# Performance work log

Hardware: AMD Instinct MI355X
Metric: run time of the kernel (lower is better)

## Reference

```python
import jax, jax.numpy as jnp
import numpy as np

N_FEATURES = 170
D_MODEL = 64
N_HEADS = 4
ALPHA = 0.1
LN_EPS = 1e-5
LEAKY_SLOPE = 0.01  # torch F.leaky_relu default
N = 3 * N_FEATURES  # 510
B = 32


def setup_inputs() -> dict:
    key = jax.random.key(0)
    ks = jax.random.split(key, 10)
    D, H = D_MODEL, N_HEADS
    s = 1.0 / np.sqrt(D)
    return {
        "x": jax.random.normal(ks[0], (B, N, D), dtype=jnp.float32),
        "causal_graph": jax.random.uniform(ks[1], (N, N), dtype=jnp.float32),
        # nn.Linear(d_model, d_model*n_heads, bias=False): stored here as (D, H*D) for x @ W
        "W": jax.random.uniform(ks[2], (D, H * D), jnp.float32, -s, s),
        "attention_w": jax.random.normal(ks[3], (H, 2 * D), dtype=jnp.float32),
        # Conv2d(2, n_heads, 3, padding=1): OIHW kernel
        "conv_w": jax.random.uniform(ks[4], (H, 2, 3, 3), jnp.float32, -1/np.sqrt(18), 1/np.sqrt(18)),
        "conv_b": jax.random.uniform(ks[5], (H,), jnp.float32, -1/np.sqrt(18), 1/np.sqrt(18)),
        # nn.Linear(d_model, 2*d_model): stored as (D, 2D)
        "fcg_w": jax.random.uniform(ks[6], (D, 2 * D), jnp.float32, -s, s),
        "fcg_b": jax.random.uniform(ks[7], (2 * D,), jnp.float32, -s, s),
        "ln_g": jnp.ones((D,), jnp.float32),
        "ln_b": jnp.zeros((D,), jnp.float32),
    }


def reference(x, causal_graph, W, attention_w, conv_w, conv_b, fcg_w, fcg_b, ln_g, ln_b):
    Bz, Nn, D = x.shape
    H = N_HEADS
    # shared projection: (B, N, H, D)
    xt = (x @ W).reshape(Bz, Nn, H, D)
    # GAT-style additive scores: concat-dot decomposed into two dot products
    w1, w2 = attention_w[:, :D], attention_w[:, D:]  # each (H, D)
    s_i = jnp.einsum('bnhd,hd->bhn', xt, w1)  # source term
    s_j = jnp.einsum('bnhd,hd->bhn', xt, w2)  # target term
    e = s_i[:, :, :, None] + s_j[:, :, None, :]  # (B, H, N, N)
    A_eva = jnp.where(e >= 0, e, LEAKY_SLOPE * e)  # leaky_relu
    # fuse mean attention with causal graph via 3x3 conv
    A_mean = A_eva.mean(axis=1)  # (B, N, N)
    causal = jnp.broadcast_to(causal_graph[None], (Bz, Nn, Nn))
    stacked = jnp.stack([A_mean, causal], axis=1)  # (B, 2, N, N)
    A_st = jax.lax.conv_general_dilated(
        stacked, conv_w, window_strides=(1, 1), padding=((1, 1), (1, 1)),
        dimension_numbers=('NCHW', 'OIHW', 'NCHW'))
    A_st = A_st + conv_b[None, :, None, None]  # (B, H, N, N)
    A = jax.nn.softmax(ALPHA * A_eva + (1.0 - ALPHA) * A_st, axis=-1)
    # multi-head aggregation then head-mean
    out = jnp.einsum('bhnm,bmhd->bnhd', A, xt).mean(axis=2)  # (B, N, D)
    # GLU
    g = out @ fcg_w + fcg_b  # (B, N, 2D)
    a, b = g[..., :D], g[..., D:]
    glu = a * jax.nn.sigmoid(b)
    # residual + layernorm
    y = glu + x
    mu = y.mean(axis=-1, keepdims=True)
    var = ((y - mu) ** 2).mean(axis=-1, keepdims=True)
    y = (y - mu) * jax.lax.rsqrt(var + LN_EPS) * ln_g + ln_b
    return y, A
```

## Files before the change

### kernel.cpp

```cpp
#include <hip/hip_runtime.h>

#define Bz 32
#define Nn 510
#define Dd 64
#define Hh 4
#define HD_ 256
#define Kpad 512
#define ALPHA_ 0.1f
#define LNEPS 1e-5f
#define SLOPE 0.01f
#define NEG_INF -3.0e38f

typedef __attribute__((ext_vector_type(8))) short short8;
typedef __attribute__((ext_vector_type(4))) float floatx4;

__device__ inline float wredsum(float v) {
  #pragma unroll
  for (int off = 32; off; off >>= 1) v += __shfl_xor(v, off, 64);
  return v;
}
__device__ inline float wredmax(float v) {
  #pragma unroll
  for (int off = 32; off; off >>= 1) v = fmaxf(v, __shfl_xor(v, off, 64));
  return v;
}
__device__ inline unsigned short f2bf(float f) {
  unsigned int u = __float_as_uint(f);
  unsigned int r = (u + 0x7fffu + ((u >> 16) & 1u)) >> 16;
  return (unsigned short)r;
}

__global__ __launch_bounds__(256) void k1_xt(const float* __restrict__ x,
                                             const float* __restrict__ W,
                                             const float* __restrict__ attw,
                                             unsigned short* __restrict__ xtT,
                                             float* __restrict__ si,
                                             float* __restrict__ sj) {
  __shared__ float Wl[64][68];
  __shared__ float xr[32][68];
  __shared__ unsigned short st[64 * 33];
  const int t = threadIdx.x;
  const int rt = blockIdx.x;
  const int b = blockIdx.y;
  const int ch = blockIdx.z;
  #pragma unroll
  for (int k = 0; k < 4; k++) {
    int f = t + k * 256;
    int kr = f >> 4;
    int c = (f & 15) * 4;
    *(float4*)&Wl[kr][c] = *(const float4*)&W[kr * HD_ + ch * 64 + c];
  }
  #pragma unroll
  for (int k = 0; k < 2; k++) {
    int f = t + k * 256;
    int r = f >> 4;
    int c = (f & 15) * 4;
    int row = rt * 32 + r;
    float4 v = make_float4(0.f, 0.f, 0.f, 0.f);
    if (row < Nn) v = *(const float4*)&x[(b * Nn + row) * Dd + c];
    *(float4*)&xr[r][c] = v;
  }
  __syncthreads();
  const int tg = t >> 4;
  const int tc = t & 15;
  const int rb = tg * 2, c0 = tc * 4;
  float acc[2][4] = {};
  #pragma unroll
  for (int k4 = 0; k4 < 16; k4++) {
    float4 xv0 = *(float4*)&xr[rb][k4 * 4];
    float4 xv1 = *(float4*)&xr[rb + 1][k4 * 4];
    #pragma unroll
    for (int kk = 0; kk < 4; kk++) {
      float4 wv = *(float4*)&Wl[k4 * 4 + kk][c0];
      float xs0 = (&xv0.x)[kk];
      float xs1 = (&xv1.x)[kk];
      acc[0][0] = fmaf(xs0, wv.x, acc[0][0]);
      acc[0][1] = fmaf(xs0, wv.y, acc[0][1]);
      acc[0][2] = fmaf(xs0, wv.z, acc[0][2]);
      acc[0][3] = fmaf(xs0, wv.w, acc[0][3]);
      acc[1][0] = fmaf(xs1, wv.x, acc[1][0]);
      acc[1][1] = fmaf(xs1, wv.y, acc[1][1]);
      acc[1][2] = fmaf(xs1, wv.z, acc[1][2]);
      acc[1][3] = fmaf(xs1, wv.w, acc[1][3]);
    }
  }
  #pragma unroll
  for (int cc = 0; cc < 4; cc++) {
    #pragma unroll
    for (int r = 0; r < 2; r++) {
      st[(c0 + cc) * 33 + rb + r] = f2bf(acc[r][cc]);
    }
  }
  float w1v[4], w2v[4];
  #pragma unroll
  for (int cc = 0; cc < 4; cc++) {
    w1v[cc] = attw[ch * 128 + c0 + cc];
    w2v[cc] = attw[ch * 128 + 64 + c0 + cc];
  }
  #pragma unroll
  for (int r = 0; r < 2; r++) {
    float p1 = acc[r][0] * w1v[0] + acc[r][1] * w1v[1] +
               acc[r][2] * w1v[2] + acc[r][3] * w1v[3];
    float p2 = acc[r][0] * w2v[0] + acc[r][1] * w2v[1] +
               acc[r][2] * w2v[2] + acc[r][3] * w2v[3];
    #pragma unroll
    for (int off = 1; off <= 8; off <<= 1) {
      p1 += __shfl_xor(p1, off, 64);
      p2 += __shfl_xor(p2, off, 64);
    }
    if (tc == 0) {
      int row = rt * 32 + rb + r;
      if (row < Nn) {
        si[(b * 4 + ch) * Nn + row] = p1;
        sj[(b * 4 + ch) * Nn + row] = p2;
      }
    }
  }
  __syncthreads();
  if (t < 64) {
    unsigned short* dst = &xtT[((size_t)(b * 4 + ch) * 64 + t) * Kpad + rt * 32];
    #pragma unroll
    for (int q = 0; q < 4; q++) {
      short8 v;
      #pragma unroll
      for (int k = 0; k < 8; k++) v[k] = (short)st[t * 33 + q * 8 + k];
      *(short8*)&dst[q * 8] = v;
    }
  }
}

__global__ __launch_bounds__(256) void k2_attn(const float* __restrict__ si,
                                               const float* __restrict__ sj,
                                               const float* __restrict__ causal,
                                               const float* __restrict__ convw,
                                               const float* __restrict__ convb,
                                               float* __restrict__ A) {
  __shared__ float am_t[10 * 8 * 68];
  __shared__ float cz_t[10 * 8 * 68];
  __shared__ float sjl[4 * 8 * 68];
  __shared__ float sil[4][12];
  const int t = threadIdx.x;
  const int i0 = blockIdx.x * 8;
  const int b = blockIdx.y;
  if (t < 40) {
    int h = t / 10, r = t % 10;
    int iq = i0 + r - 1;
    sil[h][r] = (iq >= 0 && iq < Nn) ? si[(b * 4 + h) * Nn + iq] : 0.f;
  }
  if (t >= 64 && t < 224) {
    int q = t - 64;
    int r = q >> 4, rem = q & 15;
    int e = rem >> 1, side = rem & 1;
    int idx = (r * 8 + e) * 68 + side * 65;
    am_t[idx] = 0.f;
    cz_t[idx] = 0.f;
  }
  for (int f = t; f < 2048; f += 256) {
    int h = f >> 9, j = f & 511;
    float v = (j < Nn) ? sj[(b * 4 + h) * Nn + j] : 0.f;
    sjl[(h * 8 + (j & 7)) * 68 + (j >> 3) + 1] = v;
  }
  __syncthreads();
  for (int f = t; f < 5120; f += 256) {
    int r = f >> 9, j = f & 511;
    int iq = i0 + r - 1;
    float am = 0.f, cz = 0.f;
    if (iq >= 0 && iq < Nn && j < Nn) {
      float s = 0.f;
      #pragma unroll
      for (int h = 0; h < 4; h++) {
        float e2 = sil[h][r] + sjl[(h * 8 + (j & 7)) * 68 + (j >> 3) + 1];
        s += (e2 >= 0.f) ? e2 : SLOPE * e2;
      }
      am = 0.25f * s;
      cz = causal[iq * Nn + j];
    }
    int idx = (r * 8 + (j & 7)) * 68 + (j >> 3) + 1;
    am_t[idx] = am;
    cz_t[idx] = cz;
  }
  __syncthreads();
  const int w = t >> 6, L = t & 63;
  const int j0 = L * 8;
  for (int pp = w; pp < 32; pp += 4) {
    const int il = pp >> 2, h = pp & 3;
    const int i = i0 + il;
    if (i >= Nn) continue;
    const int bh = b * 4 + h;
    const float sih = sil[h][il + 1];
    float cw[18];
    #pragma unroll
    for (int q = 0; q < 18; q++) cw[q] = convw[h * 18 + q];
    const float cb = convb[h];
    float conv[8];
    #pragma unroll
    for (int e = 0; e < 8; e++) conv[e] = cb;
    #pragma unroll
    for (int r3 = 0; r3 < 3; r3++) {
      const float* ba = &am_t[((il + r3) * 8) * 68];
      const float* bc = &cz_t[((il + r3) * 8) * 68];
      float a[10], c[10];
      a[0] = ba[7 * 68 + L];
      c[0] = bc[7 * 68 + L];
      #pragma unroll
      for (int e = 0; e < 8; e++) {
        a[1 + e] = ba[e * 68 + L + 1];
        c[1 + e] = bc[e * 68 + L + 1];
      }
      a[9] = ba[0 * 68 + L + 2];
      c[9] = bc[0 * 68 + L + 2];
      float w0 = cw[r3 * 3], w1 = cw[r3 * 3 + 1], w2 = cw[r3 * 3 + 2];
      float u0 = cw[9 + r3 * 3], u1 = cw[9 + r3 * 3 + 1], u2 = cw[9 + r3 * 3 + 2];
      #pragma unroll
      for (int e = 0; e < 8; e++) {
        float cv = conv[e];
        cv = fmaf(w0, a[e], cv);
        cv = fmaf(w1, a[e + 1], cv);
        cv = fmaf(w2, a[e + 2], cv);
        cv = fmaf(u0, c[e], cv);
        cv = fmaf(u1, c[e + 1], cv);
        cv = fmaf(u2, c[e + 2], cv);
        conv[e] = cv;
      }
    }
    float v[8];
    float mx = NEG_INF;
    #pragma unroll
    for (int e = 0; e < 8; e++) {
      float ee = sih + sjl[(h * 8 + e) * 68 + L + 1];
      float l = (ee >= 0.f) ? ee : SLOPE * ee;
      float val = ALPHA_ * l + (1.0f - ALPHA_) * conv[e];
      v[e] = (j0 + e < Nn) ? val : NEG_INF;
      mx = fmaxf(mx, v[e]);
    }
    mx = wredmax(mx);
    float p[8], s = 0.f;
    #pragma unroll
    for (int e = 0; e < 8; e++) {
      p[e] = __expf(v[e] - mx);
      s += p[e];
    }
    s = wredsum(s);
    const float inv = 1.f / s;
    #pragma unroll
    for (int e = 0; e < 8; e++) p[e] *= inv;
    float* Ar = &A[((size_t)bh * Nn + i) * Nn + j0];
    *(float4*)&Ar[0] = make_float4(p[0], p[1], p[2], p[3]);
    if (L < 63) {
      *(float4*)&Ar[4] = make_float4(p[4], p[5], p[6], p[7]);
    } else {
      *(float2*)&Ar[4] = make_float2(p[4], p[5]);
    }
  }
}

__global__ __launch_bounds__(256) void k3_out(const float* __restrict__ A,
                                              const unsigned short* __restrict__ xtT,
                                              const float* __restrict__ x,
                                              const float* __restrict__ fcgw,
                                              const float* __restrict__ fcgb,
                                              const float* __restrict__ lng,
                                              const float* __restrict__ lnb,
                                              float* __restrict__ y) {
  __shared__ float ol[16][64];
  __shared__ float gl[2][128];
  const int t = threadIdx.x;
  const int n0 = blockIdx.x * 16;
  const int b = blockIdx.y;
  const int w = t >> 6, L = t & 63;
  const int quad = L >> 4, l16 = L & 15;
  const int wc = w * 16;
  const int arow = (n0 + l16 < Nn) ? (n0 + l16) : (Nn - 1);
  floatx4 acc = {0.f, 0.f, 0.f, 0.f};
  for (int h = 0; h < 4; h++) {
    const float* Ar = &A[((size_t)(b * 4 + h) * Nn + arow) * Nn];
    const unsigned short* Xr = &xtT[((size_t)(b * 4 + h) * 64 + wc + l16) * Kpad];
    #pragma unroll 4
    for (int kt = 0; kt < 16; kt++) {
      const int m = kt * 32 + quad * 8;
      float av[8];
      if (m != 504) {
        #pragma unroll
        for (int q = 0; q < 4; q++) {
          float2 v = *(const float2*)&Ar[m + q * 2];
          av[q * 2] = v.x;
          av[q * 2 + 1] = v.y;
        }
      } else {
        #pragma unroll
        for (int q = 0; q < 3; q++) {
          float2 v = *(const float2*)&Ar[m + q * 2];
          av[q * 2] = v.x;
          av[q * 2 + 1] = v.y;
        }
        av[6] = 0.f;
        av[7] = 0.f;
      }
      short8 af;
      #pragma unroll
      for (int e = 0; e < 8; e++) af[e] = (short)f2bf(av[e]);
      short8 bf = *(const short8*)&Xr[m];
      acc = __builtin_amdgcn_mfma_f32_16x16x32_bf16(af, bf, acc, 0, 0, 0);
    }
  }
  #pragma unroll
  for (int reg = 0; reg < 4; reg++) {
    ol[quad * 4 + reg][wc + l16] = 0.25f * acc[reg];
  }
  __syncthreads();
  const int kk = t & 127;
  const int rg = t >> 7;
  for (int it = 0; it < 8; it++) {
    const int r = it * 2 + rg;
    const int row = n0 + r;
    float g = fcgb[kk];
    #pragma unroll
    for (int d = 0; d < 64; d++) g = fmaf(ol[r][d], fcgw[d * 128 + kk], g);
    gl[rg][kk] = g;
    __syncthreads();
    if (kk < 64 && row < Nn) {
      float a = gl[rg][kk];
      float bb = gl[rg][kk + 64];
      float glu = a / (1.f + __expf(-bb));
      float yv = glu + x[(b * Nn + row) * Dd + kk];
      float mu = wredsum(yv) * (1.f / 64.f);
      float dv = yv - mu;
      float var = wredsum(dv * dv) * (1.f / 64.f);
      float o = dv * rsqrtf(var + LNEPS) * lng[kk] + lnb[kk];
      y[(b * Nn + row) * Dd + kk] = o;
    }
    __syncthreads();
  }
}

extern "C" void kernel_launch(void* const* d_in, const int* in_sizes, int n_in,
                              void* d_out, int out_size, void* d_ws, size_t ws_size,
                              hipStream_t stream) {
  const float* x      = (const float*)d_in[0];
  const float* causal = (const float*)d_in[1];
  const float* W      = (const float*)d_in[2];
  const float* attw   = (const float*)d_in[3];
  const float* convw  = (const float*)d_in[4];
  const float* convb  = (const float*)d_in[5];
  const float* fcgw   = (const float*)d_in[6];
  const float* fcgb   = (const float*)d_in[7];
  const float* lng    = (const float*)d_in[8];
  const float* lnb    = (const float*)d_in[9];

  float* ws = (float*)d_ws;
  float* si = ws;
  float* sj = si + (size_t)Bz * Hh * Nn;
  unsigned short* xtT = (unsigned short*)(sj + (size_t)Bz * Hh * Nn + 16);

  float* yout = (float*)d_out;
  float* Aout = yout + (size_t)Bz * Nn * Dd;

  k1_xt  <<<dim3(16, Bz, 4), 256, 0, stream>>>(x, W, attw, xtT, si, sj);
  k2_attn<<<dim3(64, Bz), 256, 0, stream>>>(si, sj, causal, convw, convb, Aout);
  k3_out <<<dim3(32, Bz), 256, 0, stream>>>(Aout, xtT, x, fcgw, fcgb, lng, lnb, yout);
}
```

Baseline: 293.1 us.

## Stage A tiles in shared memory with double buffering in output kernel

Before, each of the four waves in k3_out read the same 16 rows of A from global memory and converted them to bf16 on its own. Now the block loads each 16x64 A chunk once, converts it, stores it into a double-buffered LDS tile and shares it across waves, with the next chunk staged while the current one feeds the MFMAs. This cuts redundant global loads and conversions of A by four times, at the cost of an LDS round trip and a __syncthreads per chunk.

```diff
diff --git a/kernel.cpp b/kernel.cpp
--- a/kernel.cpp
+++ b/kernel.cpp
@@ -262,6 +262,7 @@
                                               const float* __restrict__ lng,
                                               const float* __restrict__ lnb,
                                               float* __restrict__ y) {
+  __shared__ unsigned short Asub[2][16 * 72];
   __shared__ float ol[16][64];
   __shared__ float gl[2][128];
   const int t = threadIdx.x;
@@ -270,39 +271,50 @@
   const int w = t >> 6, L = t & 63;
   const int quad = L >> 4, l16 = L & 15;
   const int wc = w * 16;
-  const int arow = (n0 + l16 < Nn) ? (n0 + l16) : (Nn - 1);
+  const int ar = t >> 4;
+  const int amc = (t & 15) * 4;
+  const int nrow = n0 + ar;
   floatx4 acc = {0.f, 0.f, 0.f, 0.f};
-  for (int h = 0; h < 4; h++) {
-    const float* Ar = &A[((size_t)(b * 4 + h) * Nn + arow) * Nn];
-    const unsigned short* Xr = &xtT[((size_t)(b * 4 + h) * 64 + wc + l16) * Kpad];
-    #pragma unroll 4
-    for (int kt = 0; kt < 16; kt++) {
-      const int m = kt * 32 + quad * 8;
-      float av[8];
-      if (m != 504) {
+
+  auto stage = [&](int p) {
+    const int h = p >> 3;
+    const int m = (p & 7) * 64 + amc;
+    float av[4] = {0.f, 0.f, 0.f, 0.f};
+    if (nrow < Nn) {
+      const float* src = &A[((size_t)(b * 4 + h) * Nn + nrow) * Nn + m];
+      if (m + 3 < Nn) {
+        float2 v0 = *(const float2*)&src[0];
+        float2 v1 = *(const float2*)&src[2];
+        av[0] = v0.x; av[1] = v0.y; av[2] = v1.x; av[3] = v1.y;
+      } else {
+        int lim = Nn - m;
         #pragma unroll
-        for (int q = 0; q < 4; q++) {
-          float2 v = *(const float2*)&Ar[m + q * 2];
-          av[q * 2] = v.x;
-          av[q * 2 + 1] = v.y;
-        }
-      } else {
-        #pragma unroll
-        for (int q = 0; q < 3; q++) {
-          float2 v = *(const float2*)&Ar[m + q * 2];
-          av[q * 2] = v.x;
-          av[q * 2 + 1] = v.y;
-        }
-        av[6] = 0.f;
-        av[7] = 0.f;
-      }
-      short8 af;
-      #pragma unroll
-      for (int e = 0; e < 8; e++) af[e] = (short)f2bf(av[e]);
-      short8 bf = *(const short8*)&Xr[m];
-      acc = __builtin_amdgcn_mfma_f32_16x16x32_bf16(af, bf, acc, 0, 0, 0);
-    }
-  }
+        for (int q = 0; q < 4; q++) if (q < lim) av[q] = src[q];
+      }
+    }
+    ushort4 u;
+    u.x = f2bf(av[0]); u.y = f2bf(av[1]);
+    u.z = f2bf(av[2]); u.w = f2bf(av[3]);
+    *(ushort4*)&Asub[p & 1][ar * 72 + amc] = u;
+  };
+
+  stage(0);
+  __syncthreads();
+  #pragma unroll 2
+  for (int p = 0; p < 32; p++) {
+    if (p + 1 < 32) stage(p + 1);
+    const int h = p >> 3;
+    const unsigned short* Xr =
+        &xtT[((size_t)(b * 4 + h) * 64 + wc + l16) * Kpad + (p & 7) * 64];
+    short8 af0 = *(short8*)&Asub[p & 1][l16 * 72 + quad * 8];
+    short8 bf0 = *(const short8*)&Xr[quad * 8];
+    acc = __builtin_amdgcn_mfma_f32_16x16x32_bf16(af0, bf0, acc, 0, 0, 0);
+    short8 af1 = *(short8*)&Asub[p & 1][l16 * 72 + 32 + quad * 8];
+    short8 bf1 = *(const short8*)&Xr[32 + quad * 8];
+    acc = __builtin_amdgcn_mfma_f32_16x16x32_bf16(af1, bf1, acc, 0, 0, 0);
+    __syncthreads();
+  }
+
   #pragma unroll
   for (int reg = 0; reg < 4; reg++) {
     ol[quad * 4 + reg][wc + l16] = 0.25f * acc[reg];
```

Result: faster. 274.0 us (-6.5%).
